# Kernel optimization log

Hardware: AMD Instinct MI355X
Metric: run time of the kernel (lower is better)

Reference implementation:

```python
import jax, jax.numpy as jnp
import numpy as np

B, Q = 4096, 1024   # batch, time-series length
L, K = 64, 32       # num shapelets, shapelet length


def setup_inputs() -> dict:
    key = jax.random.key(0)
    k1, k2, k3, k4 = jax.random.split(key, 4)
    return {
        "ts": jax.random.normal(k1, (B, Q), dtype=jnp.float32),
        "shapelets": jax.random.normal(k2, (L, K), dtype=jnp.float32),
        "fc_w": jax.random.normal(k3, (2, L), dtype=jnp.float32) * 0.1,
        "fc_b": jax.random.normal(k4, (2,), dtype=jnp.float32) * 0.1,
    }


def reference(ts, shapelets, fc_w, fc_b):
    # Sliding-window mean squared distance, fused via the expansion
    #   mean((seg - s)^2) = (sum seg^2 - 2 seg.s + sum s^2) / K
    # which avoids materializing [B, L, S, K] windows.
    S = Q - K + 1  # number of segments

    # sliding sum of ts^2 over windows of length K -> [B, S]
    cs = jnp.concatenate([jnp.zeros((B, 1), ts.dtype), jnp.cumsum(ts * ts, axis=1)], axis=1)
    win_sq = cs[:, K:] - cs[:, :-K]

    # cross-correlation ts * shapelet -> [B, L, S] via a 1D valid conv
    cross = jax.lax.conv_general_dilated(
        ts[:, None, :],          # [B, 1, Q]  (NCW)
        shapelets[:, None, :],   # [L, 1, K]  (OIW)
        window_strides=(1,),
        padding="VALID",
        dimension_numbers=("NCW", "OIW", "NCW"),
    )

    shap_sq = jnp.sum(shapelets * shapelets, axis=1)  # [L]

    # [B, L, S] distance profile, then hard min over segment positions -> [B, L]
    dist = (win_sq[:, None, :] - 2.0 * cross + shap_sq[None, :, None]) / K
    feat = jnp.min(dist, axis=2)

    # fc1
    return feat @ fc_w.T + fc_b
```

## Files before the change

kernel.cpp:

```cpp
#include <hip/hip_runtime.h>
#include <stdint.h>

#define NB 4096
#define QLEN 1024
#define NL 64
#define KLEN 32
#define NS (QLEN - KLEN + 1)
#define WSLICE 1856

typedef __attribute__((ext_vector_type(8))) _Float16 half8;
typedef __attribute__((ext_vector_type(4))) float f32x4;

union fragh { uint32_t u[4]; half8 v; };

static __device__ __forceinline__ uint32_t pkh(float a, float b) {
    return __builtin_bit_cast(uint32_t, __builtin_amdgcn_cvt_pkrtz(a, b));
}
static __device__ __forceinline__ float lo16f(uint32_t w) {
    return (float)__builtin_bit_cast(_Float16, (unsigned short)(w & 0xFFFFu));
}
static __device__ __forceinline__ float hi16f(uint32_t w) {
    return (float)__builtin_bit_cast(_Float16, (unsigned short)(w >> 16));
}
static __device__ __forceinline__ uint32_t pkh_rne(float a, float b) {
    unsigned short ha = __builtin_bit_cast(unsigned short, (_Float16)a);
    unsigned short hb = __builtin_bit_cast(unsigned short, (_Float16)b);
    return (uint32_t)ha | ((uint32_t)hb << 16);
}

__global__ __launch_bounds__(256, 4) void shapelet_r12(
    const float* __restrict__ ts,
    const float* __restrict__ shapelets,
    const float* __restrict__ fc_w,
    const float* __restrict__ fc_b,
    float* __restrict__ out)
{
    __shared__ __align__(16) uint32_t lds[4 * WSLICE];

    const int tid  = threadIdx.x;
    const int wave = tid >> 6;
    const int lane = tid & 63;
    const int col  = lane & 15;
    const int kg   = lane >> 4;
    const int row  = blockIdx.x * 4 + wave;

    uint32_t* pkE = lds + wave * WSLICE;
    uint32_t* pkO = pkE + 528;
    uint32_t* nwh = pkO + 528;
    float*    s4  = reinterpret_cast<float*>(nwh + 512);

    const float* rowp = ts + (size_t)row * QLEN;
    float4 v[4];
    #pragma unroll
    for (int c = 0; c < 4; ++c)
        v[c] = reinterpret_cast<const float4*>(rowp)[64 * c + lane];
    float x4[4];
    #pragma unroll
    for (int c = 0; c < 4; ++c) {
        const int p = 256 * c + 4 * lane + 4;
        x4[c] = (p < QLEN) ? rowp[p] : 0.0f;
    }
    #pragma unroll
    for (int c = 0; c < 4; ++c) {
        uint2 pe = { pkh(v[c].x, v[c].y), pkh(v[c].z, v[c].w) };
        uint2 po = { pkh(v[c].y, v[c].z), pkh(v[c].w, x4[c]) };
        reinterpret_cast<uint2*>(pkE)[64 * c + lane] = pe;
        reinterpret_cast<uint2*>(pkO)[64 * c + lane] = po;
        s4[64 * c + lane] =
            fmaf(v[c].x, v[c].x, fmaf(v[c].y, v[c].y, fmaf(v[c].z, v[c].z, v[c].w * v[c].w)));
    }
    if (lane < 16) { pkE[512 + lane] = 0u; pkO[512 + lane] = 0u; }
    if (lane < 8)  s4[256 + lane] = 0.0f;

    fragh Bh[4];
    float ssq[4];
    #pragma unroll
    for (int lt = 0; lt < 4; ++lt) {
        const float* sp = shapelets + (lt * 16 + col) * KLEN + kg * 8;
        float4 f0 = *reinterpret_cast<const float4*>(sp);
        float4 f1 = *reinterpret_cast<const float4*>(sp + 4);
        Bh[lt].u[0] = pkh(f0.x, f0.y);
        Bh[lt].u[1] = pkh(f0.z, f0.w);
        Bh[lt].u[2] = pkh(f1.x, f1.y);
        Bh[lt].u[3] = pkh(f1.z, f1.w);
        float s = f0.x * f0.x;
        s = fmaf(f0.y, f0.y, s); s = fmaf(f0.z, f0.z, s); s = fmaf(f0.w, f0.w, s);
        s = fmaf(f1.x, f1.x, s); s = fmaf(f1.y, f1.y, s);
        s = fmaf(f1.z, f1.z, s); s = fmaf(f1.w, f1.w, s);
        ssq[lt] = s;
    }

    __builtin_amdgcn_wave_barrier();

    #pragma unroll
    for (int c = 0; c < 4; ++c) {
        const int q = 64 * c + lane;
        float s_[8];
        #pragma unroll
        for (int j = 0; j < 8; ++j) s_[j] = s4[q + j];
        float w0 = ((s_[0] + s_[1]) + (s_[2] + s_[3])) + ((s_[4] + s_[5]) + (s_[6] + s_[7]));
        uint32_t cw0 = pkE[2 * (q + 8)];
        uint32_t cw1 = pkE[2 * (q + 8) + 1];
        float x32 = lo16f(cw0), x33 = hi16f(cw0), x34 = lo16f(cw1);
        float w1 = fmaf(x32, x32, fmaf(-v[c].x, v[c].x, w0));
        float w2 = fmaf(x33, x33, fmaf(-v[c].y, v[c].y, w1));
        float w3 = fmaf(x34, x34, fmaf(-v[c].z, v[c].z, w2));
        const int p0 = 4 * q;
        float c0 = (p0 + 0 < NS) ? -0.5f * w0 : -60000.0f;
        float c1 = (p0 + 1 < NS) ? -0.5f * w1 : -60000.0f;
        float c2 = (p0 + 2 < NS) ? -0.5f * w2 : -60000.0f;
        float c3 = (p0 + 3 < NS) ? -0.5f * w3 : -60000.0f;
        const int qq = p0 & 31;
        const int W = ((p0 >> 5) << 4) + (((qq & 15) >> 2) << 2) + ((qq >> 4) << 1);
        uint2 hw = { pkh_rne(c0, c1), pkh_rne(c2, c3) };
        *reinterpret_cast<uint2*>(&nwh[W]) = hw;
    }

    __builtin_amdgcn_wave_barrier();

    float rmax[4][4];
    #pragma unroll
    for (int lt = 0; lt < 4; ++lt)
        #pragma unroll
        for (int e = 0; e < 4; ++e) rmax[lt][e] = -3.0e38f;

    const int par = col & 1;
    const uint32_t* apk = (par ? pkO : pkE) + (((col - par) >> 1) + kg * 4);
    const int nwb = 4 * kg;

    #pragma unroll 2
    for (int i = 0; i < 32; ++i) {
        const uint32_t* ap = apk + 16 * i;
        fragh Aa, Ab;
        #pragma unroll
        for (int j = 0; j < 4; ++j) Aa.u[j] = ap[j];
        #pragma unroll
        for (int j = 0; j < 4; ++j) Ab.u[j] = ap[8 + j];

        uint4 nw = *reinterpret_cast<const uint4*>(&nwh[16 * i + nwb]);
        f32x4 ia, ib;
        ia[0] = lo16f(nw.x); ia[1] = hi16f(nw.x);
        ia[2] = lo16f(nw.y); ia[3] = hi16f(nw.y);
        ib[0] = lo16f(nw.z); ib[1] = hi16f(nw.z);
        ib[2] = lo16f(nw.w); ib[3] = hi16f(nw.w);

        #pragma unroll
        for (int lt = 0; lt < 4; ++lt) {
            f32x4 aa = __builtin_amdgcn_mfma_f32_16x16x32_f16(Aa.v, Bh[lt].v, ia, 0, 0, 0);
            f32x4 ab = __builtin_amdgcn_mfma_f32_16x16x32_f16(Ab.v, Bh[lt].v, ib, 0, 0, 0);
            #pragma unroll
            for (int e = 0; e < 4; ++e)
                rmax[lt][e] = fmaxf(fmaxf(aa[e], ab[e]), rmax[lt][e]);
        }
    }

    float p0v = 0.0f, p1v = 0.0f;
    #pragma unroll
    for (int lt = 0; lt < 4; ++lt) {
        float m = fmaxf(fmaxf(rmax[lt][0], rmax[lt][1]),
                        fmaxf(rmax[lt][2], rmax[lt][3]));
        m = fmaxf(m, __shfl_xor(m, 16, 64));
        m = fmaxf(m, __shfl_xor(m, 32, 64));
        float sq = ssq[lt];
        sq += __shfl_xor(sq, 16, 64);
        sq += __shfl_xor(sq, 32, 64);
        float f = (sq - 2.0f * m) * (1.0f / (float)KLEN);
        p0v = fmaf(f, fc_w[lt * 16 + col], p0v);
        p1v = fmaf(f, fc_w[NL + lt * 16 + col], p1v);
    }
    #pragma unroll
    for (int off = 1; off <= 8; off <<= 1) {
        p0v += __shfl_xor(p0v, off, 64);
        p1v += __shfl_xor(p1v, off, 64);
    }
    if (lane == 0) {
        out[(size_t)row * 2 + 0] = p0v + fc_b[0];
        out[(size_t)row * 2 + 1] = p1v + fc_b[1];
    }
}

extern "C" void kernel_launch(void* const* d_in, const int* in_sizes, int n_in,
                              void* d_out, int out_size, void* d_ws, size_t ws_size,
                              hipStream_t stream) {
    const float* ts        = (const float*)d_in[0];
    const float* shapelets = (const float*)d_in[1];
    const float* fc_w      = (const float*)d_in[2];
    const float* fc_b      = (const float*)d_in[3];
    float* out = (float*)d_out;

    shapelet_r12<<<NB / 4, 256, 0, stream>>>(ts, shapelets, fc_w, fc_b, out);
}
```

Measured before the change: 23.80 us.

## Split each time-series row across two waves with LDS max reduction

Each row is now handled by two waves instead of one. Each wave packs half the row into shared LDS and runs the MFMA sliding-window loop over half the segments. The partial maxima are combined through a small LDS buffer behind a block barrier, and the grid doubles to 2048 blocks with a higher occupancy hint. The aim is more parallelism and shorter per-wave critical paths, at the cost of block-wide syncs and duplicated shapelet fragment loads per wave.

```diff
diff --git a/kernel.cpp b/kernel.cpp
--- a/kernel.cpp
+++ b/kernel.cpp
@@ -6,7 +6,7 @@
 #define NL 64
 #define KLEN 32
 #define NS (QLEN - KLEN + 1)
-#define WSLICE 1856
+#define SLICE 1856
 
 typedef __attribute__((ext_vector_type(8))) _Float16 half8;
 typedef __attribute__((ext_vector_type(4))) float f32x4;
@@ -28,49 +28,54 @@
     return (uint32_t)ha | ((uint32_t)hb << 16);
 }
 
-__global__ __launch_bounds__(256, 4) void shapelet_r12(
+__global__ __launch_bounds__(256, 8) void shapelet_r13(
     const float* __restrict__ ts,
     const float* __restrict__ shapelets,
     const float* __restrict__ fc_w,
     const float* __restrict__ fc_b,
     float* __restrict__ out)
 {
-    __shared__ __align__(16) uint32_t lds[4 * WSLICE];
+    __shared__ __align__(16) uint32_t lds[2 * SLICE];
+    __shared__ float lds_pm[2][2][NL];
 
     const int tid  = threadIdx.x;
+    const int lane = tid & 63;
     const int wave = tid >> 6;
-    const int lane = tid & 63;
+    const int rw   = wave >> 1;
+    const int h    = wave & 1;
     const int col  = lane & 15;
     const int kg   = lane >> 4;
-    const int row  = blockIdx.x * 4 + wave;
-
-    uint32_t* pkE = lds + wave * WSLICE;
+    const int row  = blockIdx.x * 2 + rw;
+
+    uint32_t* pkE = lds + rw * SLICE;
     uint32_t* pkO = pkE + 528;
     uint32_t* nwh = pkO + 528;
     float*    s4  = reinterpret_cast<float*>(nwh + 512);
 
     const float* rowp = ts + (size_t)row * QLEN;
-    float4 v[4];
-    #pragma unroll
-    for (int c = 0; c < 4; ++c)
-        v[c] = reinterpret_cast<const float4*>(rowp)[64 * c + lane];
-    float x4[4];
-    #pragma unroll
-    for (int c = 0; c < 4; ++c) {
-        const int p = 256 * c + 4 * lane + 4;
-        x4[c] = (p < QLEN) ? rowp[p] : 0.0f;
-    }
-    #pragma unroll
-    for (int c = 0; c < 4; ++c) {
-        uint2 pe = { pkh(v[c].x, v[c].y), pkh(v[c].z, v[c].w) };
-        uint2 po = { pkh(v[c].y, v[c].z), pkh(v[c].w, x4[c]) };
-        reinterpret_cast<uint2*>(pkE)[64 * c + lane] = pe;
-        reinterpret_cast<uint2*>(pkO)[64 * c + lane] = po;
-        s4[64 * c + lane] =
-            fmaf(v[c].x, v[c].x, fmaf(v[c].y, v[c].y, fmaf(v[c].z, v[c].z, v[c].w * v[c].w)));
-    }
-    if (lane < 16) { pkE[512 + lane] = 0u; pkO[512 + lane] = 0u; }
-    if (lane < 8)  s4[256 + lane] = 0.0f;
+    float4 v0, v1;
+    {
+        v0 = reinterpret_cast<const float4*>(rowp)[64 * (2 * h + 0) + lane];
+        v1 = reinterpret_cast<const float4*>(rowp)[64 * (2 * h + 1) + lane];
+        const int pa = 256 * (2 * h + 0) + 4 * lane + 4;
+        const int pb = 256 * (2 * h + 1) + 4 * lane + 4;
+        float xa = rowp[pa];
+        float xb = (pb < QLEN) ? rowp[pb] : 0.0f;
+        uint2 pe0 = { pkh(v0.x, v0.y), pkh(v0.z, v0.w) };
+        uint2 po0 = { pkh(v0.y, v0.z), pkh(v0.w, xa) };
+        uint2 pe1 = { pkh(v1.x, v1.y), pkh(v1.z, v1.w) };
+        uint2 po1 = { pkh(v1.y, v1.z), pkh(v1.w, xb) };
+        reinterpret_cast<uint2*>(pkE)[64 * (2 * h + 0) + lane] = pe0;
+        reinterpret_cast<uint2*>(pkO)[64 * (2 * h + 0) + lane] = po0;
+        reinterpret_cast<uint2*>(pkE)[64 * (2 * h + 1) + lane] = pe1;
+        reinterpret_cast<uint2*>(pkO)[64 * (2 * h + 1) + lane] = po1;
+        s4[64 * (2 * h + 0) + lane] =
+            fmaf(v0.x, v0.x, fmaf(v0.y, v0.y, fmaf(v0.z, v0.z, v0.w * v0.w)));
+        s4[64 * (2 * h + 1) + lane] =
+            fmaf(v1.x, v1.x, fmaf(v1.y, v1.y, fmaf(v1.z, v1.z, v1.w * v1.w)));
+    }
+    if (h == 1 && lane < 16) { pkE[512 + lane] = 0u; pkO[512 + lane] = 0u; }
+    if (h == 1 && lane < 8)  s4[256 + lane] = 0.0f;
 
     fragh Bh[4];
     float ssq[4];
@@ -90,11 +95,12 @@
         ssq[lt] = s;
     }
 
-    __builtin_amdgcn_wave_barrier();
-
-    #pragma unroll
-    for (int c = 0; c < 4; ++c) {
-        const int q = 64 * c + lane;
+    __syncthreads();
+
+    #pragma unroll
+    for (int cc = 0; cc < 2; ++cc) {
+        const int q  = 64 * (2 * h + cc) + lane;
+        const float4 vv = cc ? v1 : v0;
         float s_[8];
         #pragma unroll
         for (int j = 0; j < 8; ++j) s_[j] = s4[q + j];
@@ -102,9 +108,9 @@
         uint32_t cw0 = pkE[2 * (q + 8)];
         uint32_t cw1 = pkE[2 * (q + 8) + 1];
         float x32 = lo16f(cw0), x33 = hi16f(cw0), x34 = lo16f(cw1);
-        float w1 = fmaf(x32, x32, fmaf(-v[c].x, v[c].x, w0));
-        float w2 = fmaf(x33, x33, fmaf(-v[c].y, v[c].y, w1));
-        float w3 = fmaf(x34, x34, fmaf(-v[c].z, v[c].z, w2));
+        float w1 = fmaf(x32, x32, fmaf(-vv.x, vv.x, w0));
+        float w2 = fmaf(x33, x33, fmaf(-vv.y, vv.y, w1));
+        float w3 = fmaf(x34, x34, fmaf(-vv.z, vv.z, w2));
         const int p0 = 4 * q;
         float c0 = (p0 + 0 < NS) ? -0.5f * w0 : -60000.0f;
         float c1 = (p0 + 1 < NS) ? -0.5f * w1 : -60000.0f;
@@ -125,11 +131,11 @@
         for (int e = 0; e < 4; ++e) rmax[lt][e] = -3.0e38f;
 
     const int par = col & 1;
-    const uint32_t* apk = (par ? pkO : pkE) + (((col - par) >> 1) + kg * 4);
-    const int nwb = 4 * kg;
+    const uint32_t* apk = (par ? pkO : pkE) + (((col - par) >> 1) + kg * 4) + 256 * h;
+    const uint32_t* nwp = nwh + 256 * h + 4 * kg;
 
     #pragma unroll 2
-    for (int i = 0; i < 32; ++i) {
+    for (int i = 0; i < 16; ++i) {
         const uint32_t* ap = apk + 16 * i;
         fragh Aa, Ab;
         #pragma unroll
@@ -137,7 +143,7 @@
         #pragma unroll
         for (int j = 0; j < 4; ++j) Ab.u[j] = ap[8 + j];
 
-        uint4 nw = *reinterpret_cast<const uint4*>(&nwh[16 * i + nwb]);
+        uint4 nw = *reinterpret_cast<const uint4*>(nwp + 16 * i);
         f32x4 ia, ib;
         ia[0] = lo16f(nw.x); ia[1] = hi16f(nw.x);
         ia[2] = lo16f(nw.y); ia[3] = hi16f(nw.y);
@@ -154,28 +160,38 @@
         }
     }
 
-    float p0v = 0.0f, p1v = 0.0f;
     #pragma unroll
     for (int lt = 0; lt < 4; ++lt) {
         float m = fmaxf(fmaxf(rmax[lt][0], rmax[lt][1]),
                         fmaxf(rmax[lt][2], rmax[lt][3]));
         m = fmaxf(m, __shfl_xor(m, 16, 64));
         m = fmaxf(m, __shfl_xor(m, 32, 64));
-        float sq = ssq[lt];
-        sq += __shfl_xor(sq, 16, 64);
-        sq += __shfl_xor(sq, 32, 64);
-        float f = (sq - 2.0f * m) * (1.0f / (float)KLEN);
-        p0v = fmaf(f, fc_w[lt * 16 + col], p0v);
-        p1v = fmaf(f, fc_w[NL + lt * 16 + col], p1v);
-    }
-    #pragma unroll
-    for (int off = 1; off <= 8; off <<= 1) {
-        p0v += __shfl_xor(p0v, off, 64);
-        p1v += __shfl_xor(p1v, off, 64);
-    }
-    if (lane == 0) {
-        out[(size_t)row * 2 + 0] = p0v + fc_b[0];
-        out[(size_t)row * 2 + 1] = p1v + fc_b[1];
+        if (kg == 0) lds_pm[rw][h][lt * 16 + col] = m;
+    }
+    __syncthreads();
+
+    if (h == 0) {
+        float p0v = 0.0f, p1v = 0.0f;
+        #pragma unroll
+        for (int lt = 0; lt < 4; ++lt) {
+            const int ft = lt * 16 + col;
+            float m = fmaxf(lds_pm[rw][0][ft], lds_pm[rw][1][ft]);
+            float sq = ssq[lt];
+            sq += __shfl_xor(sq, 16, 64);
+            sq += __shfl_xor(sq, 32, 64);
+            float f = (sq - 2.0f * m) * (1.0f / (float)KLEN);
+            p0v = fmaf(f, fc_w[ft], p0v);
+            p1v = fmaf(f, fc_w[NL + ft], p1v);
+        }
+        #pragma unroll
+        for (int off = 1; off <= 8; off <<= 1) {
+            p0v += __shfl_xor(p0v, off, 64);
+            p1v += __shfl_xor(p1v, off, 64);
+        }
+        if (lane == 0) {
+            out[(size_t)row * 2 + 0] = p0v + fc_b[0];
+            out[(size_t)row * 2 + 1] = p1v + fc_b[1];
+        }
     }
 }
 
@@ -188,5 +204,5 @@
     const float* fc_b      = (const float*)d_in[3];
     float* out = (float*)d_out;
 
-    shapelet_r12<<<NB / 4, 256, 0, stream>>>(ts, shapelets, fc_w, fc_b, out);
-}
+    shapelet_r13<<<NB / 2, 256, 0, stream>>>(ts, shapelets, fc_w, fc_b, out);
+}
```

Result: slower. 27.98 us (+17.6%).

## Split each row's shapelets across two waves and reduce partials in second kernel

Applied to the files above, without the earlier changes.

Each time-series row is now handled by two waves, each computing MFMA distances for half of the shapelets (two 16-wide tiles instead of four). Blocks cover two rows, the grid doubles, and launch bounds allow 8 blocks per CU, with fewer accumulators per thread. The goal is more parallelism and better latency hiding. In exchange, both waves of a row redundantly load the row and write identical LDS staging data without a block barrier. Partial FC outputs go to a workspace, and a second small kernel sums them and adds the bias, which adds a launch.

```diff
diff --git a/kernel.cpp b/kernel.cpp
--- a/kernel.cpp
+++ b/kernel.cpp
@@ -6,7 +6,7 @@
 #define NL 64
 #define KLEN 32
 #define NS (QLEN - KLEN + 1)
-#define WSLICE 1856
+#define SLICE 1840
 
 typedef __attribute__((ext_vector_type(8))) _Float16 half8;
 typedef __attribute__((ext_vector_type(4))) float f32x4;
@@ -28,66 +28,61 @@
     return (uint32_t)ha | ((uint32_t)hb << 16);
 }
 
-__global__ __launch_bounds__(256, 4) void shapelet_r12(
+__global__ __launch_bounds__(256, 8) void shapelet_r14(
     const float* __restrict__ ts,
     const float* __restrict__ shapelets,
     const float* __restrict__ fc_w,
-    const float* __restrict__ fc_b,
-    float* __restrict__ out)
+    float* __restrict__ ws)
 {
-    __shared__ __align__(16) uint32_t lds[4 * WSLICE];
+    __shared__ __align__(16) uint32_t lds[2 * SLICE];
 
     const int tid  = threadIdx.x;
+    const int lane = tid & 63;
     const int wave = tid >> 6;
-    const int lane = tid & 63;
+    const int rw   = wave >> 1;
+    const int h    = wave & 1;
     const int col  = lane & 15;
     const int kg   = lane >> 4;
-    const int row  = blockIdx.x * 4 + wave;
-
-    uint32_t* pkE = lds + wave * WSLICE;
+    const int row  = blockIdx.x * 2 + rw;
+
+    uint32_t* pkE = lds + rw * SLICE;
     uint32_t* pkO = pkE + 528;
     uint32_t* nwh = pkO + 528;
     float*    s4  = reinterpret_cast<float*>(nwh + 512);
 
     const float* rowp = ts + (size_t)row * QLEN;
-    float4 v[4];
-    #pragma unroll
-    for (int c = 0; c < 4; ++c)
-        v[c] = reinterpret_cast<const float4*>(rowp)[64 * c + lane];
-    float x4[4];
     #pragma unroll
     for (int c = 0; c < 4; ++c) {
+        float4 v = reinterpret_cast<const float4*>(rowp)[64 * c + lane];
         const int p = 256 * c + 4 * lane + 4;
-        x4[c] = (p < QLEN) ? rowp[p] : 0.0f;
-    }
-    #pragma unroll
-    for (int c = 0; c < 4; ++c) {
-        uint2 pe = { pkh(v[c].x, v[c].y), pkh(v[c].z, v[c].w) };
-        uint2 po = { pkh(v[c].y, v[c].z), pkh(v[c].w, x4[c]) };
+        float x4 = (p < QLEN) ? rowp[p] : 0.0f;
+        uint2 pe = { pkh(v.x, v.y), pkh(v.z, v.w) };
+        uint2 po = { pkh(v.y, v.z), pkh(v.w, x4) };
         reinterpret_cast<uint2*>(pkE)[64 * c + lane] = pe;
         reinterpret_cast<uint2*>(pkO)[64 * c + lane] = po;
         s4[64 * c + lane] =
-            fmaf(v[c].x, v[c].x, fmaf(v[c].y, v[c].y, fmaf(v[c].z, v[c].z, v[c].w * v[c].w)));
+            fmaf(v.x, v.x, fmaf(v.y, v.y, fmaf(v.z, v.z, v.w * v.w)));
     }
     if (lane < 16) { pkE[512 + lane] = 0u; pkO[512 + lane] = 0u; }
     if (lane < 8)  s4[256 + lane] = 0.0f;
 
-    fragh Bh[4];
-    float ssq[4];
-    #pragma unroll
-    for (int lt = 0; lt < 4; ++lt) {
+    fragh Bh[2];
+    float ssq[2];
+    #pragma unroll
+    for (int t = 0; t < 2; ++t) {
+        const int lt = 2 * h + t;
         const float* sp = shapelets + (lt * 16 + col) * KLEN + kg * 8;
         float4 f0 = *reinterpret_cast<const float4*>(sp);
         float4 f1 = *reinterpret_cast<const float4*>(sp + 4);
-        Bh[lt].u[0] = pkh(f0.x, f0.y);
-        Bh[lt].u[1] = pkh(f0.z, f0.w);
-        Bh[lt].u[2] = pkh(f1.x, f1.y);
-        Bh[lt].u[3] = pkh(f1.z, f1.w);
+        Bh[t].u[0] = pkh(f0.x, f0.y);
+        Bh[t].u[1] = pkh(f0.z, f0.w);
+        Bh[t].u[2] = pkh(f1.x, f1.y);
+        Bh[t].u[3] = pkh(f1.z, f1.w);
         float s = f0.x * f0.x;
         s = fmaf(f0.y, f0.y, s); s = fmaf(f0.z, f0.z, s); s = fmaf(f0.w, f0.w, s);
         s = fmaf(f1.x, f1.x, s); s = fmaf(f1.y, f1.y, s);
         s = fmaf(f1.z, f1.z, s); s = fmaf(f1.w, f1.w, s);
-        ssq[lt] = s;
+        ssq[t] = s;
     }
 
     __builtin_amdgcn_wave_barrier();
@@ -99,12 +94,15 @@
         #pragma unroll
         for (int j = 0; j < 8; ++j) s_[j] = s4[q + j];
         float w0 = ((s_[0] + s_[1]) + (s_[2] + s_[3])) + ((s_[4] + s_[5]) + (s_[6] + s_[7]));
+        uint32_t a0  = pkE[2 * q];
+        uint32_t a1  = pkE[2 * q + 1];
         uint32_t cw0 = pkE[2 * (q + 8)];
         uint32_t cw1 = pkE[2 * (q + 8) + 1];
+        float x0  = lo16f(a0),  x1  = hi16f(a0),  x2  = lo16f(a1);
         float x32 = lo16f(cw0), x33 = hi16f(cw0), x34 = lo16f(cw1);
-        float w1 = fmaf(x32, x32, fmaf(-v[c].x, v[c].x, w0));
-        float w2 = fmaf(x33, x33, fmaf(-v[c].y, v[c].y, w1));
-        float w3 = fmaf(x34, x34, fmaf(-v[c].z, v[c].z, w2));
+        float w1 = fmaf(x32, x32, fmaf(-x0, x0, w0));
+        float w2 = fmaf(x33, x33, fmaf(-x1, x1, w1));
+        float w3 = fmaf(x34, x34, fmaf(-x2, x2, w2));
         const int p0 = 4 * q;
         float c0 = (p0 + 0 < NS) ? -0.5f * w0 : -60000.0f;
         float c1 = (p0 + 1 < NS) ? -0.5f * w1 : -60000.0f;
@@ -118,11 +116,11 @@
 
     __builtin_amdgcn_wave_barrier();
 
-    float rmax[4][4];
-    #pragma unroll
-    for (int lt = 0; lt < 4; ++lt)
-        #pragma unroll
-        for (int e = 0; e < 4; ++e) rmax[lt][e] = -3.0e38f;
+    float rmax[2][4];
+    #pragma unroll
+    for (int t = 0; t < 2; ++t)
+        #pragma unroll
+        for (int e = 0; e < 4; ++e) rmax[t][e] = -3.0e38f;
 
     const int par = col & 1;
     const uint32_t* apk = (par ? pkO : pkE) + (((col - par) >> 1) + kg * 4);
@@ -145,28 +143,29 @@
         ib[2] = lo16f(nw.w); ib[3] = hi16f(nw.w);
 
         #pragma unroll
-        for (int lt = 0; lt < 4; ++lt) {
-            f32x4 aa = __builtin_amdgcn_mfma_f32_16x16x32_f16(Aa.v, Bh[lt].v, ia, 0, 0, 0);
-            f32x4 ab = __builtin_amdgcn_mfma_f32_16x16x32_f16(Ab.v, Bh[lt].v, ib, 0, 0, 0);
+        for (int t = 0; t < 2; ++t) {
+            f32x4 aa = __builtin_amdgcn_mfma_f32_16x16x32_f16(Aa.v, Bh[t].v, ia, 0, 0, 0);
+            f32x4 ab = __builtin_amdgcn_mfma_f32_16x16x32_f16(Ab.v, Bh[t].v, ib, 0, 0, 0);
             #pragma unroll
             for (int e = 0; e < 4; ++e)
-                rmax[lt][e] = fmaxf(fmaxf(aa[e], ab[e]), rmax[lt][e]);
+                rmax[t][e] = fmaxf(fmaxf(aa[e], ab[e]), rmax[t][e]);
         }
     }
 
     float p0v = 0.0f, p1v = 0.0f;
     #pragma unroll
-    for (int lt = 0; lt < 4; ++lt) {
-        float m = fmaxf(fmaxf(rmax[lt][0], rmax[lt][1]),
-                        fmaxf(rmax[lt][2], rmax[lt][3]));
+    for (int t = 0; t < 2; ++t) {
+        const int ft = (2 * h + t) * 16 + col;
+        float m = fmaxf(fmaxf(rmax[t][0], rmax[t][1]),
+                        fmaxf(rmax[t][2], rmax[t][3]));
         m = fmaxf(m, __shfl_xor(m, 16, 64));
         m = fmaxf(m, __shfl_xor(m, 32, 64));
-        float sq = ssq[lt];
+        float sq = ssq[t];
         sq += __shfl_xor(sq, 16, 64);
         sq += __shfl_xor(sq, 32, 64);
         float f = (sq - 2.0f * m) * (1.0f / (float)KLEN);
-        p0v = fmaf(f, fc_w[lt * 16 + col], p0v);
-        p1v = fmaf(f, fc_w[NL + lt * 16 + col], p1v);
+        p0v = fmaf(f, fc_w[ft], p0v);
+        p1v = fmaf(f, fc_w[NL + ft], p1v);
     }
     #pragma unroll
     for (int off = 1; off <= 8; off <<= 1) {
@@ -174,8 +173,19 @@
         p1v += __shfl_xor(p1v, off, 64);
     }
     if (lane == 0) {
-        out[(size_t)row * 2 + 0] = p0v + fc_b[0];
-        out[(size_t)row * 2 + 1] = p1v + fc_b[1];
+        ws[(size_t)row * 4 + 2 * h + 0] = p0v;
+        ws[(size_t)row * 4 + 2 * h + 1] = p1v;
+    }
+}
+
+__global__ __launch_bounds__(256) void shapelet_fin(
+    const float* __restrict__ ws, const float* __restrict__ fc_b,
+    float* __restrict__ out)
+{
+    const int idx = blockIdx.x * 256 + threadIdx.x;
+    if (idx < 2 * NB) {
+        const int row = idx >> 1, c = idx & 1;
+        out[idx] = ws[4 * row + c] + ws[4 * row + 2 + c] + fc_b[c];
     }
 }
 
@@ -187,6 +197,8 @@
     const float* fc_w      = (const float*)d_in[2];
     const float* fc_b      = (const float*)d_in[3];
     float* out = (float*)d_out;
-
-    shapelet_r12<<<NB / 4, 256, 0, stream>>>(ts, shapelets, fc_w, fc_b, out);
-}
+    float* ws  = (float*)d_ws;
+
+    shapelet_r14<<<NB / 2, 256, 0, stream>>>(ts, shapelets, fc_w, ws);
+    shapelet_fin<<<(2 * NB + 255) / 256, 256, 0, stream>>>(ws, fc_b, out);
+}
```

New measurement: 29.50 us. 23.9% more time.

## Switch sliding-window MFMA from 16x16x32 to 32x32x16 f16 tiles

Applied to the files above, without the earlier changes.

Replaces the 16x16x32 f16 MFMA tiling with 32x32x16 MFMAs that cover 32 shapelets per tile and split K=32 into two chained halves. The LDS fragment layout, window-norm init layout and reductions are reworked to match, and the loop is no longer unrolled. The aim is fewer MFMA issues and fewer cross-lane shuffles per output, at the cost of 32 accumulator registers per lane for the running max and longer dependent MFMA chains.

```diff
diff --git a/kernel.cpp b/kernel.cpp
--- a/kernel.cpp
+++ b/kernel.cpp
@@ -6,12 +6,12 @@
 #define NL 64
 #define KLEN 32
 #define NS (QLEN - KLEN + 1)
-#define WSLICE 1856
+#define WSLICE 1864
 
-typedef __attribute__((ext_vector_type(8))) _Float16 half8;
-typedef __attribute__((ext_vector_type(4))) float f32x4;
+typedef __attribute__((ext_vector_type(8)))  _Float16 half8;
+typedef __attribute__((ext_vector_type(16))) float    f32x16;
 
-union fragh { uint32_t u[4]; half8 v; };
+union frag4 { uint4 q; half8 v; uint32_t u[4]; };
 
 static __device__ __forceinline__ uint32_t pkh(float a, float b) {
     return __builtin_bit_cast(uint32_t, __builtin_amdgcn_cvt_pkrtz(a, b));
@@ -28,7 +28,7 @@
     return (uint32_t)ha | ((uint32_t)hb << 16);
 }
 
-__global__ __launch_bounds__(256, 4) void shapelet_r12(
+__global__ __launch_bounds__(256, 4) void shapelet_r20(
     const float* __restrict__ ts,
     const float* __restrict__ shapelets,
     const float* __restrict__ fc_w,
@@ -40,21 +40,21 @@
     const int tid  = threadIdx.x;
     const int wave = tid >> 6;
     const int lane = tid & 63;
-    const int col  = lane & 15;
-    const int kg   = lane >> 4;
+    const int l31  = lane & 31;
+    const int hk   = lane >> 5;
     const int row  = blockIdx.x * 4 + wave;
 
     uint32_t* pkE = lds + wave * WSLICE;
-    uint32_t* pkO = pkE + 528;
-    uint32_t* nwh = pkO + 528;
+    uint32_t* pkO = pkE + 544;
+    uint32_t* nwh = pkO + 544;
     float*    s4  = reinterpret_cast<float*>(nwh + 512);
 
     const float* rowp = ts + (size_t)row * QLEN;
     float4 v[4];
+    float  x4[4];
     #pragma unroll
     for (int c = 0; c < 4; ++c)
         v[c] = reinterpret_cast<const float4*>(rowp)[64 * c + lane];
-    float x4[4];
     #pragma unroll
     for (int c = 0; c < 4; ++c) {
         const int p = 256 * c + 4 * lane + 4;
@@ -69,24 +69,28 @@
         s4[64 * c + lane] =
             fmaf(v[c].x, v[c].x, fmaf(v[c].y, v[c].y, fmaf(v[c].z, v[c].z, v[c].w * v[c].w)));
     }
-    if (lane < 16) { pkE[512 + lane] = 0u; pkO[512 + lane] = 0u; }
+    if (lane < 32) { pkE[512 + lane] = 0u; pkO[512 + lane] = 0u; }
     if (lane < 8)  s4[256 + lane] = 0.0f;
 
-    fragh Bh[4];
-    float ssq[4];
+    frag4 Bf[2][2];
+    float ssq[2];
     #pragma unroll
-    for (int lt = 0; lt < 4; ++lt) {
-        const float* sp = shapelets + (lt * 16 + col) * KLEN + kg * 8;
-        float4 f0 = *reinterpret_cast<const float4*>(sp);
-        float4 f1 = *reinterpret_cast<const float4*>(sp + 4);
-        Bh[lt].u[0] = pkh(f0.x, f0.y);
-        Bh[lt].u[1] = pkh(f0.z, f0.w);
-        Bh[lt].u[2] = pkh(f1.x, f1.y);
-        Bh[lt].u[3] = pkh(f1.z, f1.w);
-        float s = f0.x * f0.x;
-        s = fmaf(f0.y, f0.y, s); s = fmaf(f0.z, f0.z, s); s = fmaf(f0.w, f0.w, s);
-        s = fmaf(f1.x, f1.x, s); s = fmaf(f1.y, f1.y, s);
-        s = fmaf(f1.z, f1.z, s); s = fmaf(f1.w, f1.w, s);
+    for (int lt = 0; lt < 2; ++lt) {
+        float s = 0.0f;
+        #pragma unroll
+        for (int kh = 0; kh < 2; ++kh) {
+            const float* sp = shapelets + (lt * 32 + l31) * KLEN + kh * 16 + hk * 8;
+            float4 f0 = *reinterpret_cast<const float4*>(sp);
+            float4 f1 = *reinterpret_cast<const float4*>(sp + 4);
+            Bf[lt][kh].u[0] = pkh(f0.x, f0.y);
+            Bf[lt][kh].u[1] = pkh(f0.z, f0.w);
+            Bf[lt][kh].u[2] = pkh(f1.x, f1.y);
+            Bf[lt][kh].u[3] = pkh(f1.z, f1.w);
+            s = fmaf(f0.x, f0.x, s); s = fmaf(f0.y, f0.y, s);
+            s = fmaf(f0.z, f0.z, s); s = fmaf(f0.w, f0.w, s);
+            s = fmaf(f1.x, f1.x, s); s = fmaf(f1.y, f1.y, s);
+            s = fmaf(f1.z, f1.z, s); s = fmaf(f1.w, f1.w, s);
+        }
         ssq[lt] = s;
     }
 
@@ -110,66 +114,69 @@
         float c1 = (p0 + 1 < NS) ? -0.5f * w1 : -60000.0f;
         float c2 = (p0 + 2 < NS) ? -0.5f * w2 : -60000.0f;
         float c3 = (p0 + 3 < NS) ? -0.5f * w3 : -60000.0f;
-        const int qq = p0 & 31;
-        const int W = ((p0 >> 5) << 4) + (((qq & 15) >> 2) << 2) + ((qq >> 4) << 1);
+        const int W = 16 * (p0 >> 5) + ((p0 >> 2) & 1) * 8 + ((p0 >> 3) & 3) * 2;
         uint2 hw = { pkh_rne(c0, c1), pkh_rne(c2, c3) };
         *reinterpret_cast<uint2*>(&nwh[W]) = hw;
     }
 
     __builtin_amdgcn_wave_barrier();
 
-    float rmax[4][4];
+    float rmax[2][16];
     #pragma unroll
-    for (int lt = 0; lt < 4; ++lt)
+    for (int lt = 0; lt < 2; ++lt)
         #pragma unroll
-        for (int e = 0; e < 4; ++e) rmax[lt][e] = -3.0e38f;
+        for (int e = 0; e < 16; ++e) rmax[lt][e] = -3.0e38f;
 
-    const int par = col & 1;
-    const uint32_t* apk = (par ? pkO : pkE) + (((col - par) >> 1) + kg * 4);
-    const int nwb = 4 * kg;
+    const int par = l31 & 1;
+    const uint32_t* apk = (par ? pkO : pkE) + (((l31 - par) >> 1) + hk * 4);
+    const int nwb = hk * 8;
 
-    #pragma unroll 2
-    for (int i = 0; i < 32; ++i) {
-        const uint32_t* ap = apk + 16 * i;
-        fragh Aa, Ab;
+    #pragma unroll 1
+    for (int t = 0; t < 32; ++t) {
+        const uint32_t* ap = apk + 16 * t;
+        frag4 A1, A2;
         #pragma unroll
-        for (int j = 0; j < 4; ++j) Aa.u[j] = ap[j];
+        for (int j = 0; j < 4; ++j) A1.u[j] = ap[j];
         #pragma unroll
-        for (int j = 0; j < 4; ++j) Ab.u[j] = ap[8 + j];
+        for (int j = 0; j < 4; ++j) A2.u[j] = ap[8 + j];
+        uint4 nw0 = *reinterpret_cast<const uint4*>(&nwh[16 * t + nwb]);
+        uint4 nw1 = *reinterpret_cast<const uint4*>(&nwh[16 * t + nwb + 4]);
 
-        uint4 nw = *reinterpret_cast<const uint4*>(&nwh[16 * i + nwb]);
-        f32x4 ia, ib;
-        ia[0] = lo16f(nw.x); ia[1] = hi16f(nw.x);
-        ia[2] = lo16f(nw.y); ia[3] = hi16f(nw.y);
-        ib[0] = lo16f(nw.z); ib[1] = hi16f(nw.z);
-        ib[2] = lo16f(nw.w); ib[3] = hi16f(nw.w);
+        f32x16 init;
+        init[0]  = lo16f(nw0.x); init[1]  = hi16f(nw0.x);
+        init[2]  = lo16f(nw0.y); init[3]  = hi16f(nw0.y);
+        init[4]  = lo16f(nw0.z); init[5]  = hi16f(nw0.z);
+        init[6]  = lo16f(nw0.w); init[7]  = hi16f(nw0.w);
+        init[8]  = lo16f(nw1.x); init[9]  = hi16f(nw1.x);
+        init[10] = lo16f(nw1.y); init[11] = hi16f(nw1.y);
+        init[12] = lo16f(nw1.z); init[13] = hi16f(nw1.z);
+        init[14] = lo16f(nw1.w); init[15] = hi16f(nw1.w);
+
+        f32x16 a0 = __builtin_amdgcn_mfma_f32_32x32x16_f16(A1.v, Bf[0][0].v, init, 0, 0, 0);
+        a0        = __builtin_amdgcn_mfma_f32_32x32x16_f16(A2.v, Bf[0][1].v, a0,   0, 0, 0);
+        f32x16 a1 = __builtin_amdgcn_mfma_f32_32x32x16_f16(A1.v, Bf[1][0].v, init, 0, 0, 0);
+        a1        = __builtin_amdgcn_mfma_f32_32x32x16_f16(A2.v, Bf[1][1].v, a1,   0, 0, 0);
 
         #pragma unroll
-        for (int lt = 0; lt < 4; ++lt) {
-            f32x4 aa = __builtin_amdgcn_mfma_f32_16x16x32_f16(Aa.v, Bh[lt].v, ia, 0, 0, 0);
-            f32x4 ab = __builtin_amdgcn_mfma_f32_16x16x32_f16(Ab.v, Bh[lt].v, ib, 0, 0, 0);
-            #pragma unroll
-            for (int e = 0; e < 4; ++e)
-                rmax[lt][e] = fmaxf(fmaxf(aa[e], ab[e]), rmax[lt][e]);
-        }
+        for (int e = 0; e < 16; ++e) rmax[0][e] = fmaxf(rmax[0][e], a0[e]);
+        #pragma unroll
+        for (int e = 0; e < 16; ++e) rmax[1][e] = fmaxf(rmax[1][e], a1[e]);
     }
 
     float p0v = 0.0f, p1v = 0.0f;
     #pragma unroll
-    for (int lt = 0; lt < 4; ++lt) {
-        float m = fmaxf(fmaxf(rmax[lt][0], rmax[lt][1]),
-                        fmaxf(rmax[lt][2], rmax[lt][3]));
-        m = fmaxf(m, __shfl_xor(m, 16, 64));
+    for (int lt = 0; lt < 2; ++lt) {
+        float m = rmax[lt][0];
+        #pragma unroll
+        for (int e = 1; e < 16; ++e) m = fmaxf(m, rmax[lt][e]);
         m = fmaxf(m, __shfl_xor(m, 32, 64));
-        float sq = ssq[lt];
-        sq += __shfl_xor(sq, 16, 64);
-        sq += __shfl_xor(sq, 32, 64);
+        float sq = ssq[lt] + __shfl_xor(ssq[lt], 32, 64);
         float f = (sq - 2.0f * m) * (1.0f / (float)KLEN);
-        p0v = fmaf(f, fc_w[lt * 16 + col], p0v);
-        p1v = fmaf(f, fc_w[NL + lt * 16 + col], p1v);
+        p0v = fmaf(f, fc_w[lt * 32 + l31], p0v);
+        p1v = fmaf(f, fc_w[NL + lt * 32 + l31], p1v);
     }
     #pragma unroll
-    for (int off = 1; off <= 8; off <<= 1) {
+    for (int off = 1; off <= 16; off <<= 1) {
         p0v += __shfl_xor(p0v, off, 64);
         p1v += __shfl_xor(p1v, off, 64);
     }
@@ -188,5 +195,5 @@
     const float* fc_b      = (const float*)d_in[3];
     float* out = (float*)d_out;
 
-    shapelet_r12<<<NB / 4, 256, 0, stream>>>(ts, shapelets, fc_w, fc_b, out);
+    shapelet_r20<<<NB / 4, 256, 0, stream>>>(ts, shapelets, fc_w, fc_b, out);
 }
```

Result: slower. 39.14 us (+64.5%).
